# Kernel optimization log

Hardware: AMD Instinct MI355X
Metric: run time of the kernel (lower is better)

Reference implementation:

```python
import jax, jax.numpy as jnp
import numpy as np

N_NODES = 50000
N_EDGES = 800000
D_FEAT = 128
HEADS = 8
UNITS = 32
LEAKY_ALPHA = 0.2  # tf.nn.leaky_relu default
EPS = 1e-7


def setup_inputs() -> dict:
    key = jax.random.key(0)
    k1, k2, k3, k4, k5 = jax.random.split(key, 5)
    x = jax.random.normal(k1, (N_NODES, D_FEAT), dtype=jnp.float32)
    edges = jax.random.randint(k2, (N_EDGES, 2), 0, N_NODES, dtype=jnp.int32)
    kernel = jax.random.normal(k3, (D_FEAT, HEADS * UNITS), dtype=jnp.float32) * (1.0 / np.sqrt(D_FEAT))
    ka1 = jax.random.normal(k4, (1, HEADS, UNITS), dtype=jnp.float32) * (1.0 / np.sqrt(UNITS))
    ka2 = jax.random.normal(k5, (1, HEADS, UNITS), dtype=jnp.float32) * (1.0 / np.sqrt(UNITS))
    bias = jnp.zeros((HEADS * UNITS,), dtype=jnp.float32)
    return {"x": x, "edges": edges, "kernel": kernel, "ka1": ka1, "ka2": ka2, "bias": bias}


def reference(x, edges, kernel, ka1, ka2, bias):
    # x: [N, F]; edges: [E, 2] with columns (source, target)
    n_nodes = x.shape[0]
    targets = edges[:, 1]
    sources = edges[:, 0]

    h = (x @ kernel).reshape(-1, HEADS, UNITS)  # [N, H, U]

    f_t = jnp.sum(h * ka1, axis=-1)[targets]  # [E, H]
    # Faithful to source: f_s gathers from the EDGE-level f_t by source ids
    # (original code overwrites the ka2-based node scores), so ka2 is unused.
    f_s = f_t[sources]  # [E, H]

    scores = jax.nn.leaky_relu(f_t + f_s, negative_slope=LEAKY_ALPHA)  # [E, H]
    seg_max = jax.ops.segment_max(scores, targets, num_segments=n_nodes)
    scores = jnp.exp(scores - seg_max[targets])
    denom = jax.ops.segment_sum(scores, targets, num_segments=n_nodes) + EPS
    scores = scores / denom[targets]  # segment softmax over incoming edges

    out = jax.ops.segment_sum(scores[..., None] * h[sources], targets, num_segments=n_nodes)  # [N, H, U]
    out = out.reshape(n_nodes, HEADS * UNITS)  # concat merge
    return jax.nn.elu(out + bias)
```

## Files before the change

kernel.cpp:

```cpp
#include <hip/hip_runtime.h>
#include <hip/hip_fp16.h>

#define N_NODES 50000
#define N_EDGES 800000
#define D_FEAT 128
#define HEADS 8
#define UNITS 32
#define HU (HEADS * UNITS)
#define LEAKY 0.2f
#define EPSV 1e-7f
#define NBLK 196

typedef _Float16 half8 __attribute__((ext_vector_type(8)));
typedef float f32x4 __attribute__((ext_vector_type(4)));

struct h4pk { __half2 a, b; };

#define WBLK 128
__global__ __launch_bounds__(256) void k_wt(const float* __restrict__ W,
                                            __half* __restrict__ Wt,
                                            int* __restrict__ counts) {
    const int i = blockIdx.x * 256 + threadIdx.x;
    const int n = i >> 7, k = i & 127;
    Wt[i] = __float2half(W[k * HU + n]);
    for (int j = i; j < N_NODES; j += WBLK * 256) counts[j] = 0;
}

#define GB 1563
#define CB 3125
__global__ __launch_bounds__(64, 1) void k_big(const float* __restrict__ x,
                                               const __half* __restrict__ Wt,
                                               const float* __restrict__ ka1,
                                               const int* __restrict__ edges,
                                               int* __restrict__ counts,
                                               int* __restrict__ rank,
                                               __half* __restrict__ h,
                                               float* __restrict__ f) {
    const int l = threadIdx.x;
    if (blockIdx.x >= GB) {
        const int base = (blockIdx.x - GB) * 256;
#pragma unroll
        for (int j = 0; j < 4; ++j) {
            const int e = base + j * 64 + l;
            if (e < N_EDGES) {
                const int tgt = edges[2 * e + 1];
                rank[e] = atomicAdd(&counts[tgt], 1);
            }
        }
        return;
    }
    const int row16 = l & 15, kg = l >> 4;
    const int rbase = blockIdx.x * 32;

    half8 a0[4], a1[4];
    const int r0 = min(rbase + row16, N_NODES - 1);
    const int r1 = min(rbase + 16 + row16, N_NODES - 1);
    const float* xp0 = x + (size_t)r0 * D_FEAT + kg * 8;
    const float* xp1 = x + (size_t)r1 * D_FEAT + kg * 8;
#pragma unroll
    for (int ks = 0; ks < 4; ++ks) {
        const float4 u0 = *reinterpret_cast<const float4*>(xp0 + ks * 32);
        const float4 v0 = *reinterpret_cast<const float4*>(xp0 + ks * 32 + 4);
        const float4 u1 = *reinterpret_cast<const float4*>(xp1 + ks * 32);
        const float4 v1 = *reinterpret_cast<const float4*>(xp1 + ks * 32 + 4);
        half8 t0, t1;
        t0[0] = (_Float16)u0.x; t0[1] = (_Float16)u0.y; t0[2] = (_Float16)u0.z; t0[3] = (_Float16)u0.w;
        t0[4] = (_Float16)v0.x; t0[5] = (_Float16)v0.y; t0[6] = (_Float16)v0.z; t0[7] = (_Float16)v0.w;
        t1[0] = (_Float16)u1.x; t1[1] = (_Float16)u1.y; t1[2] = (_Float16)u1.z; t1[3] = (_Float16)u1.w;
        t1[4] = (_Float16)v1.x; t1[5] = (_Float16)v1.y; t1[6] = (_Float16)v1.z; t1[7] = (_Float16)v1.w;
        a0[ks] = t0; a1[ks] = t1;
    }

    f32x4 acc0[16], acc1[16];
#pragma unroll
    for (int ct = 0; ct < 16; ++ct) {
        acc0[ct] = (f32x4){0.f, 0.f, 0.f, 0.f};
        acc1[ct] = (f32x4){0.f, 0.f, 0.f, 0.f};
    }

#pragma unroll
    for (int ct = 0; ct < 16; ++ct) {
        const __half* wp = Wt + (ct * 16 + row16) * D_FEAT + kg * 8;
#pragma unroll
        for (int ks = 0; ks < 4; ++ks) {
            const half8 bf = *reinterpret_cast<const half8*>(wp + ks * 32);
            acc0[ct] = __builtin_amdgcn_mfma_f32_16x16x32_f16(a0[ks], bf, acc0[ct], 0, 0, 0);
            acc1[ct] = __builtin_amdgcn_mfma_f32_16x16x32_f16(a1[ks], bf, acc1[ct], 0, 0, 0);
        }
    }

#pragma unroll
    for (int tile = 0; tile < 2; ++tile) {
        const int rb2 = rbase + tile * 16;
#pragma unroll
        for (int ct = 0; ct < 16; ++ct) {
            const int col = ct * 16 + row16;
            const f32x4 av = tile ? acc1[ct] : acc0[ct];
#pragma unroll
            for (int r = 0; r < 4; ++r) {
                const int hr = rb2 + kg * 4 + r;
                if (hr < N_NODES)
                    h[(size_t)hr * HU + col] = __float2half(av[r]);
            }
        }
#pragma unroll
        for (int hd = 0; hd < 8; ++hd) {
            const float ka = ka1[hd * 32 + row16];
            const float kb = ka1[hd * 32 + 16 + row16];
            const f32x4 ae = tile ? acc1[2 * hd] : acc0[2 * hd];
            const f32x4 ao = tile ? acc1[2 * hd + 1] : acc0[2 * hd + 1];
#pragma unroll
            for (int r = 0; r < 4; ++r) {
                float v = ae[r] * ka + ao[r] * kb;
                v += __shfl_xor(v, 1);
                v += __shfl_xor(v, 2);
                v += __shfl_xor(v, 4);
                v += __shfl_xor(v, 8);
                if (row16 == 0) {
                    const int hr = rb2 + kg * 4 + r;
                    if (hr < N_NODES) f[(size_t)hr * HEADS + hd] = v;
                }
            }
        }
    }
}

__global__ __launch_bounds__(256) void k_scanA(const int* __restrict__ counts,
                                               int* __restrict__ partials) {
    const int i = blockIdx.x * 256 + threadIdx.x;
    int v = (i < N_NODES) ? counts[i] : 0;
#pragma unroll
    for (int m = 32; m >= 1; m >>= 1) v += __shfl_xor(v, m);
    __shared__ int ws[4];
    if ((threadIdx.x & 63) == 0) ws[threadIdx.x >> 6] = v;
    __syncthreads();
    if (threadIdx.x == 0) partials[blockIdx.x] = ws[0] + ws[1] + ws[2] + ws[3];
}

__global__ __launch_bounds__(256) void k_scanC(const int* __restrict__ counts,
                                               const int* __restrict__ partials,
                                               const int* __restrict__ edges,
                                               const float* __restrict__ f,
                                               int* __restrict__ offs,
                                               float* __restrict__ g) {
    __shared__ int sp[256];
    __shared__ int s[256];
    const int t = threadIdx.x;

    sp[t] = (t < NBLK) ? partials[t] : 0;
    __syncthreads();
    for (int o = 1; o < 256; o <<= 1) {
        const int u = (t >= o) ? sp[t - o] : 0;
        __syncthreads();
        sp[t] += u;
        __syncthreads();
    }
    const int prefix = (blockIdx.x > 0) ? sp[blockIdx.x - 1] : 0;

    const int i = blockIdx.x * 256 + t;
    const int v = (i < N_NODES) ? counts[i] : 0;
    s[t] = v;
    __syncthreads();
    for (int o = 1; o < 256; o <<= 1) {
        const int u = (t >= o) ? s[t - o] : 0;
        __syncthreads();
        s[t] += u;
        __syncthreads();
    }
    if (i < N_NODES) {
        offs[i] = prefix + s[t] - v;
        const int t2 = edges[2 * i + 1];
        const float4 A = *reinterpret_cast<const float4*>(f + (size_t)t2 * HEADS);
        const float4 B = *reinterpret_cast<const float4*>(f + (size_t)t2 * HEADS + 4);
        *reinterpret_cast<float4*>(g + (size_t)i * HEADS) = A;
        *reinterpret_cast<float4*>(g + (size_t)i * HEADS + 4) = B;
    }
}

#define EBLK 3125
__global__ __launch_bounds__(256) void k_fill(const int* __restrict__ edges,
                                              const int* __restrict__ offs,
                                              const int* __restrict__ rank,
                                              int* __restrict__ elist) {
    const int e = blockIdx.x * 256 + threadIdx.x;
    if (e >= N_EDGES) return;
    const int2 st = reinterpret_cast<const int2*>(edges)[e];
    elist[offs[st.y] + rank[e]] = st.x;
}

__global__ __launch_bounds__(256) void k_out(const __half* __restrict__ h,
                                             const int* __restrict__ elist,
                                             const float* __restrict__ f,
                                             const float* __restrict__ g,
                                             const int* __restrict__ offs,
                                             const int* __restrict__ counts,
                                             const float* __restrict__ bias,
                                             float* __restrict__ out) {
    const int n = blockIdx.x * 4 + (threadIdx.x >> 6);
    if (n >= N_NODES) return;
    const int lane = threadIdx.x & 63;
    const int head = lane >> 3;
    const int c4 = lane * 4;
    const int start = offs[n];
    const int end = start + counts[n];
    const float fn = f[(size_t)n * HEADS + head];

    float d = 0.f;
    float4 acc = make_float4(0.f, 0.f, 0.f, 0.f);

    int p = start;
    for (; p + 8 <= end; p += 8) {
        int ss[8];
#pragma unroll
        for (int j = 0; j < 8; ++j) ss[j] = elist[p + j];
        float gz[8];
#pragma unroll
        for (int j = 0; j < 8; ++j) gz[j] = g[(size_t)ss[j] * HEADS + head];
        h4pk hv[8];
#pragma unroll
        for (int j = 0; j < 8; ++j) hv[j] = *reinterpret_cast<const h4pk*>(h + (size_t)ss[j] * HU + c4);
#pragma unroll
        for (int j = 0; j < 8; ++j) {
            float z = fn + gz[j];
            z = (z > 0.f) ? z : LEAKY * z;
            const float w = __expf(z);
            d += w;
            const float2 fa = __half22float2(hv[j].a);
            const float2 fb = __half22float2(hv[j].b);
            acc.x += w * fa.x; acc.y += w * fa.y; acc.z += w * fb.x; acc.w += w * fb.y;
        }
    }
    for (; p + 4 <= end; p += 4) {
        int ss[4];
#pragma unroll
        for (int j = 0; j < 4; ++j) ss[j] = elist[p + j];
        float gz[4];
#pragma unroll
        for (int j = 0; j < 4; ++j) gz[j] = g[(size_t)ss[j] * HEADS + head];
        h4pk hv[4];
#pragma unroll
        for (int j = 0; j < 4; ++j) hv[j] = *reinterpret_cast<const h4pk*>(h + (size_t)ss[j] * HU + c4);
#pragma unroll
        for (int j = 0; j < 4; ++j) {
            float z = fn + gz[j];
            z = (z > 0.f) ? z : LEAKY * z;
            const float w = __expf(z);
            d += w;
            const float2 fa = __half22float2(hv[j].a);
            const float2 fb = __half22float2(hv[j].b);
            acc.x += w * fa.x; acc.y += w * fa.y; acc.z += w * fb.x; acc.w += w * fb.y;
        }
    }
    for (; p < end; ++p) {
        const int s = elist[p];
        float z = fn + g[(size_t)s * HEADS + head];
        z = (z > 0.f) ? z : LEAKY * z;
        const float w = __expf(z);
        const h4pk hv = *reinterpret_cast<const h4pk*>(h + (size_t)s * HU + c4);
        const float2 fa = __half22float2(hv.a);
        const float2 fb = __half22float2(hv.b);
        d += w;
        acc.x += w * fa.x;
        acc.y += w * fa.y;
        acc.z += w * fb.x;
        acc.w += w * fb.y;
    }

    const float inv = 1.f / (d + EPSV);
    const float4 b = *reinterpret_cast<const float4*>(bias + c4);
    float v;
    float4 o;
    v = acc.x * inv + b.x; o.x = (v > 0.f) ? v : expm1f(v);
    v = acc.y * inv + b.y; o.y = (v > 0.f) ? v : expm1f(v);
    v = acc.z * inv + b.z; o.z = (v > 0.f) ? v : expm1f(v);
    v = acc.w * inv + b.w; o.w = (v > 0.f) ? v : expm1f(v);
    *reinterpret_cast<float4*>(out + (size_t)n * HU + c4) = o;
}

extern "C" void kernel_launch(void* const* d_in, const int* in_sizes, int n_in,
                              void* d_out, int out_size, void* d_ws, size_t ws_size,
                              hipStream_t stream) {
    const float* x = (const float*)d_in[0];
    const int* edges = (const int*)d_in[1];
    const float* W = (const float*)d_in[2];
    const float* ka1 = (const float*)d_in[3];
    const float* bias = (const float*)d_in[5];
    float* out = (float*)d_out;

    char* ws = (char*)d_ws;
    size_t off = 0;
    auto alloc = [&](size_t bytes) -> void* {
        void* p = ws + off;
        off = (off + bytes + 255) & ~size_t(255);
        return p;
    };
    __half* h = (__half*)alloc(sizeof(__half) * (size_t)N_NODES * HU);
    __half* Wt = (__half*)alloc(sizeof(__half) * D_FEAT * HU);
    float* f = (float*)alloc(sizeof(float) * N_NODES * HEADS);
    float* g = (float*)alloc(sizeof(float) * N_NODES * HEADS);
    int* counts = (int*)alloc(sizeof(int) * N_NODES);
    int* offs = (int*)alloc(sizeof(int) * N_NODES);
    int* partials = (int*)alloc(sizeof(int) * NBLK);
    int* rank = (int*)alloc(sizeof(int) * N_EDGES);
    int* elist = (int*)alloc(sizeof(int) * N_EDGES);

    k_wt<<<WBLK, 256, 0, stream>>>(W, Wt, counts);
    k_big<<<GB + CB, 64, 0, stream>>>(x, Wt, ka1, edges, counts, rank, h, f);
    k_scanA<<<NBLK, 256, 0, stream>>>(counts, partials);
    k_scanC<<<NBLK, 256, 0, stream>>>(counts, partials, edges, f, offs, g);
    k_fill<<<EBLK, 256, 0, stream>>>(edges, offs, rank, elist);
    k_out<<<(N_NODES + 3) / 4, 256, 0, stream>>>(h, elist, f, g, offs, counts, bias, out);
}
```

Measured before the change: 140.6 us.

## Replace two-pass scan with atomic wave offsets; widen GEMM tiles and reorder blocks

The two-kernel prefix scan over node counts becomes a single kernel: each wavefront scans its own lanes with shuffles and claims a contiguous range from a global counter with one atomic. This drops a launch and the redundant block-partials scan. Segment ranges are therefore no longer in node order, which works because only each node's offset and count are used later. The projection blocks now handle 64 rows instead of 32 so each W fragment is reused four times, at the cost of more registers. Edge-counting blocks are dispatched before the GEMM blocks.

```diff
diff --git a/kernel.cpp b/kernel.cpp
--- a/kernel.cpp
+++ b/kernel.cpp
@@ -19,15 +19,17 @@
 #define WBLK 128
 __global__ __launch_bounds__(256) void k_wt(const float* __restrict__ W,
                                             __half* __restrict__ Wt,
-                                            int* __restrict__ counts) {
+                                            int* __restrict__ counts,
+                                            int* __restrict__ gtotal) {
     const int i = blockIdx.x * 256 + threadIdx.x;
     const int n = i >> 7, k = i & 127;
     Wt[i] = __float2half(W[k * HU + n]);
     for (int j = i; j < N_NODES; j += WBLK * 256) counts[j] = 0;
-}
-
-#define GB 1563
+    if (i == 0) gtotal[0] = 0;
+}
+
 #define CB 3125
+#define GB 782
 __global__ __launch_bounds__(64, 1) void k_big(const float* __restrict__ x,
                                                const __half* __restrict__ Wt,
                                                const float* __restrict__ ka1,
@@ -37,8 +39,8 @@
                                                __half* __restrict__ h,
                                                float* __restrict__ f) {
     const int l = threadIdx.x;
-    if (blockIdx.x >= GB) {
-        const int base = (blockIdx.x - GB) * 256;
+    if (blockIdx.x < CB) {
+        const int base = blockIdx.x * 256;
 #pragma unroll
         for (int j = 0; j < 4; ++j) {
             const int e = base + j * 64 + l;
@@ -50,33 +52,29 @@
         return;
     }
     const int row16 = l & 15, kg = l >> 4;
-    const int rbase = blockIdx.x * 32;
-
-    half8 a0[4], a1[4];
-    const int r0 = min(rbase + row16, N_NODES - 1);
-    const int r1 = min(rbase + 16 + row16, N_NODES - 1);
-    const float* xp0 = x + (size_t)r0 * D_FEAT + kg * 8;
-    const float* xp1 = x + (size_t)r1 * D_FEAT + kg * 8;
-#pragma unroll
-    for (int ks = 0; ks < 4; ++ks) {
-        const float4 u0 = *reinterpret_cast<const float4*>(xp0 + ks * 32);
-        const float4 v0 = *reinterpret_cast<const float4*>(xp0 + ks * 32 + 4);
-        const float4 u1 = *reinterpret_cast<const float4*>(xp1 + ks * 32);
-        const float4 v1 = *reinterpret_cast<const float4*>(xp1 + ks * 32 + 4);
-        half8 t0, t1;
-        t0[0] = (_Float16)u0.x; t0[1] = (_Float16)u0.y; t0[2] = (_Float16)u0.z; t0[3] = (_Float16)u0.w;
-        t0[4] = (_Float16)v0.x; t0[5] = (_Float16)v0.y; t0[6] = (_Float16)v0.z; t0[7] = (_Float16)v0.w;
-        t1[0] = (_Float16)u1.x; t1[1] = (_Float16)u1.y; t1[2] = (_Float16)u1.z; t1[3] = (_Float16)u1.w;
-        t1[4] = (_Float16)v1.x; t1[5] = (_Float16)v1.y; t1[6] = (_Float16)v1.z; t1[7] = (_Float16)v1.w;
-        a0[ks] = t0; a1[ks] = t1;
-    }
-
-    f32x4 acc0[16], acc1[16];
-#pragma unroll
-    for (int ct = 0; ct < 16; ++ct) {
-        acc0[ct] = (f32x4){0.f, 0.f, 0.f, 0.f};
-        acc1[ct] = (f32x4){0.f, 0.f, 0.f, 0.f};
-    }
+    const int rbase = (blockIdx.x - CB) * 64;
+
+    half8 a[4][4];
+#pragma unroll
+    for (int tile = 0; tile < 4; ++tile) {
+        const int rr = min(rbase + tile * 16 + row16, N_NODES - 1);
+        const float* xp = x + (size_t)rr * D_FEAT + kg * 8;
+#pragma unroll
+        for (int ks = 0; ks < 4; ++ks) {
+            const float4 u = *reinterpret_cast<const float4*>(xp + ks * 32);
+            const float4 v = *reinterpret_cast<const float4*>(xp + ks * 32 + 4);
+            half8 t;
+            t[0] = (_Float16)u.x; t[1] = (_Float16)u.y; t[2] = (_Float16)u.z; t[3] = (_Float16)u.w;
+            t[4] = (_Float16)v.x; t[5] = (_Float16)v.y; t[6] = (_Float16)v.z; t[7] = (_Float16)v.w;
+            a[tile][ks] = t;
+        }
+    }
+
+    f32x4 acc[4][16];
+#pragma unroll
+    for (int tile = 0; tile < 4; ++tile)
+#pragma unroll
+        for (int ct = 0; ct < 16; ++ct) acc[tile][ct] = (f32x4){0.f, 0.f, 0.f, 0.f};
 
 #pragma unroll
     for (int ct = 0; ct < 16; ++ct) {
@@ -84,18 +82,19 @@
 #pragma unroll
         for (int ks = 0; ks < 4; ++ks) {
             const half8 bf = *reinterpret_cast<const half8*>(wp + ks * 32);
-            acc0[ct] = __builtin_amdgcn_mfma_f32_16x16x32_f16(a0[ks], bf, acc0[ct], 0, 0, 0);
-            acc1[ct] = __builtin_amdgcn_mfma_f32_16x16x32_f16(a1[ks], bf, acc1[ct], 0, 0, 0);
-        }
-    }
-
-#pragma unroll
-    for (int tile = 0; tile < 2; ++tile) {
+#pragma unroll
+            for (int tile = 0; tile < 4; ++tile)
+                acc[tile][ct] = __builtin_amdgcn_mfma_f32_16x16x32_f16(a[tile][ks], bf, acc[tile][ct], 0, 0, 0);
+        }
+    }
+
+#pragma unroll
+    for (int tile = 0; tile < 4; ++tile) {
         const int rb2 = rbase + tile * 16;
 #pragma unroll
         for (int ct = 0; ct < 16; ++ct) {
             const int col = ct * 16 + row16;
-            const f32x4 av = tile ? acc1[ct] : acc0[ct];
+            const f32x4 av = acc[tile][ct];
 #pragma unroll
             for (int r = 0; r < 4; ++r) {
                 const int hr = rb2 + kg * 4 + r;
@@ -107,8 +106,8 @@
         for (int hd = 0; hd < 8; ++hd) {
             const float ka = ka1[hd * 32 + row16];
             const float kb = ka1[hd * 32 + 16 + row16];
-            const f32x4 ae = tile ? acc1[2 * hd] : acc0[2 * hd];
-            const f32x4 ao = tile ? acc1[2 * hd + 1] : acc0[2 * hd + 1];
+            const f32x4 ae = acc[tile][2 * hd];
+            const f32x4 ao = acc[tile][2 * hd + 1];
 #pragma unroll
             for (int r = 0; r < 4; ++r) {
                 float v = ae[r] * ka + ao[r] * kb;
@@ -125,50 +124,27 @@
     }
 }
 
-__global__ __launch_bounds__(256) void k_scanA(const int* __restrict__ counts,
-                                               int* __restrict__ partials) {
+__global__ __launch_bounds__(256) void k_offs(const int* __restrict__ counts,
+                                              const int* __restrict__ edges,
+                                              const float* __restrict__ f,
+                                              int* __restrict__ offs,
+                                              float* __restrict__ g,
+                                              int* __restrict__ gtotal) {
     const int i = blockIdx.x * 256 + threadIdx.x;
-    int v = (i < N_NODES) ? counts[i] : 0;
-#pragma unroll
-    for (int m = 32; m >= 1; m >>= 1) v += __shfl_xor(v, m);
-    __shared__ int ws[4];
-    if ((threadIdx.x & 63) == 0) ws[threadIdx.x >> 6] = v;
-    __syncthreads();
-    if (threadIdx.x == 0) partials[blockIdx.x] = ws[0] + ws[1] + ws[2] + ws[3];
-}
-
-__global__ __launch_bounds__(256) void k_scanC(const int* __restrict__ counts,
-                                               const int* __restrict__ partials,
-                                               const int* __restrict__ edges,
-                                               const float* __restrict__ f,
-                                               int* __restrict__ offs,
-                                               float* __restrict__ g) {
-    __shared__ int sp[256];
-    __shared__ int s[256];
-    const int t = threadIdx.x;
-
-    sp[t] = (t < NBLK) ? partials[t] : 0;
-    __syncthreads();
-    for (int o = 1; o < 256; o <<= 1) {
-        const int u = (t >= o) ? sp[t - o] : 0;
-        __syncthreads();
-        sp[t] += u;
-        __syncthreads();
-    }
-    const int prefix = (blockIdx.x > 0) ? sp[blockIdx.x - 1] : 0;
-
-    const int i = blockIdx.x * 256 + t;
+    const int lane = threadIdx.x & 63;
     const int v = (i < N_NODES) ? counts[i] : 0;
-    s[t] = v;
-    __syncthreads();
-    for (int o = 1; o < 256; o <<= 1) {
-        const int u = (t >= o) ? s[t - o] : 0;
-        __syncthreads();
-        s[t] += u;
-        __syncthreads();
-    }
+    int inc = v;
+#pragma unroll
+    for (int o = 1; o < 64; o <<= 1) {
+        const int u = __shfl_up(inc, o);
+        if (lane >= o) inc += u;
+    }
+    const int wsum = __shfl(inc, 63);
+    int base = 0;
+    if (lane == 63 && wsum > 0) base = atomicAdd(gtotal, wsum);
+    base = __shfl(base, 63);
     if (i < N_NODES) {
-        offs[i] = prefix + s[t] - v;
+        offs[i] = base + inc - v;
         const int t2 = edges[2 * i + 1];
         const float4 A = *reinterpret_cast<const float4*>(f + (size_t)t2 * HEADS);
         const float4 B = *reinterpret_cast<const float4*>(f + (size_t)t2 * HEADS + 4);
@@ -300,14 +276,13 @@
     float* g = (float*)alloc(sizeof(float) * N_NODES * HEADS);
     int* counts = (int*)alloc(sizeof(int) * N_NODES);
     int* offs = (int*)alloc(sizeof(int) * N_NODES);
-    int* partials = (int*)alloc(sizeof(int) * NBLK);
+    int* gtotal = (int*)alloc(sizeof(int) * 64);
     int* rank = (int*)alloc(sizeof(int) * N_EDGES);
     int* elist = (int*)alloc(sizeof(int) * N_EDGES);
 
-    k_wt<<<WBLK, 256, 0, stream>>>(W, Wt, counts);
-    k_big<<<GB + CB, 64, 0, stream>>>(x, Wt, ka1, edges, counts, rank, h, f);
-    k_scanA<<<NBLK, 256, 0, stream>>>(counts, partials);
-    k_scanC<<<NBLK, 256, 0, stream>>>(counts, partials, edges, f, offs, g);
+    k_wt<<<WBLK, 256, 0, stream>>>(W, Wt, counts, gtotal);
+    k_big<<<CB + GB, 64, 0, stream>>>(x, Wt, ka1, edges, counts, rank, h, f);
+    k_offs<<<NBLK, 256, 0, stream>>>(counts, edges, f, offs, g, gtotal);
     k_fill<<<EBLK, 256, 0, stream>>>(edges, offs, rank, elist);
     k_out<<<(N_NODES + 3) / 4, 256, 0, stream>>>(h, elist, f, g, offs, counts, bias, out);
 }
```

Result: slower. 181.7 us (+29.2%).
